# Kernel tuning notes

Hardware: AMD Instinct MI355X
Metric: run time of the kernel (lower is better)

Reference implementation:

```python
import jax, jax.numpy as jnp
import numpy as np

B, NSTEP, NSAMPLE = 16, 32, 10
EMBED, STATE, VOCAB, TOTAL = 128, 512, 32000, 8192
STD_SCALE = 0.113
EPS = 1e-5


def setup_inputs() -> dict:
    key = jax.random.key(0)
    ks = jax.random.split(key, 9)
    g = lambda k, shape: jax.random.normal(k, shape, jnp.float32) * 0.05
    return {
        "zi": jax.random.randint(ks[0], (B,), 0, TOTAL),
        "y": jax.random.randint(ks[1], (B, NSTEP), 0, VOCAB),
        "rd": jax.random.uniform(ks[2], (NSTEP, B, NSAMPLE), jnp.float32),
        "latent": g(ks[3], (TOTAL, EMBED)),
        "state_pref_W": g(ks[4], (STATE, 2 * EMBED)),
        "state_pref_b": g(ks[5], (STATE,)),
        "state_move": g(ks[6], (STATE, EMBED)),
        "vocab_W": g(ks[7], (VOCAB, EMBED)),
        "vocab_b": g(ks[8], (VOCAB,)),
    }


def reference(zi, y, rd, latent, state_pref_W, state_pref_b, state_move, vocab_W, vocab_b):
    # z: [B, NSAMPLE, D] -- latent row per batch element, repeated over samples
    z0 = jnp.repeat(latent[zi][:, None, :], NSAMPLE, axis=1)

    def step(carry, rd_t):
        z, zold, lp = carry
        # per-step normalization (torch std is unbiased, ddof=1)
        z = z / (EPS + jnp.std(z, axis=-1, ddof=1, keepdims=True)) * STD_SCALE
        pref = jnp.concatenate([zold, z], axis=-1) @ state_pref_W.T + state_pref_b  # [B,S,STATE]
        xp = jax.nn.softmax(pref, axis=-1)
        xpc = jnp.cumsum(xp, axis=-1)
        # first index where rd < cumulative prob (argmax of bool = first True)
        which = jnp.argmax(rd_t[:, :, None] < xpc, axis=-1)  # [B,S]
        xps = jnp.take_along_axis(xp, which[:, :, None], axis=-1)[..., 0]
        lp = lp + jnp.log(xps)
        mvs = state_move[which]  # [B,S,D]
        return (z + mvs, z, mvs), mvs

    init = (z0, jnp.zeros_like(z0), jnp.zeros((B, NSAMPLE), jnp.float32))
    # note: carry slot 2 of init is lp=0; fix tuple to match step outputs
    init = (z0, jnp.zeros_like(z0), jnp.zeros((B, NSAMPLE), jnp.float32))

    def step_fixed(carry, rd_t):
        z, zold, lp = carry
        z = z / (EPS + jnp.std(z, axis=-1, ddof=1, keepdims=True)) * STD_SCALE
        pref = jnp.concatenate([zold, z], axis=-1) @ state_pref_W.T + state_pref_b
        xp = jax.nn.softmax(pref, axis=-1)
        xpc = jnp.cumsum(xp, axis=-1)
        which = jnp.argmax(rd_t[:, :, None] < xpc, axis=-1)
        xps = jnp.take_along_axis(xp, which[:, :, None], axis=-1)[..., 0]
        lp = lp + jnp.log(xps)
        mvs = state_move[which]
        return (z + mvs, z, lp), mvs

    (_, _, lp), emits = jax.lax.scan(step_fixed, init, rd)  # emits: [T,B,S,D]
    emits = jnp.transpose(emits, (1, 0, 2, 3))  # [B,T,S,D]
    ys = jax.nn.log_softmax(emits @ vocab_W.T + vocab_b, axis=-1)  # [B,T,S,V]
    idx = jnp.broadcast_to(y[:, :, None, None], (B, NSTEP, NSAMPLE, 1))
    yp = jnp.take_along_axis(ys, idx, axis=-1)[..., 0]  # [B,T,S]
    return yp.mean(axis=2)  # [B,T]
```

## Files before the change

### kernel.cpp

```cpp
#include <hip/hip_runtime.h>
#include <hip/hip_bf16.h>

#define B_ 16
#define T_ 32
#define NS_ 10
#define D_ 128
#define ST_ 512
#define V_ 32000
#define NCHAIN 160

using short8  = __attribute__((ext_vector_type(8))) short;
using f32x4   = __attribute__((ext_vector_type(4))) float;
using half8   = __attribute__((ext_vector_type(8))) _Float16;
using half2v  = __attribute__((ext_vector_type(2))) _Float16;

__device__ __forceinline__ unsigned short f2bf(float f){
  unsigned u = __float_as_uint(f);
  u += 0x7FFFu + ((u >> 16) & 1u);
  return (unsigned short)(u >> 16);
}
__device__ __forceinline__ unsigned packbf(float a, float b){
  return ((unsigned)f2bf(b) << 16) | (unsigned)f2bf(a);
}
__device__ __forceinline__ unsigned short f2h(float f){
  return __builtin_bit_cast(unsigned short, (_Float16)f);
}
__device__ __forceinline__ float h2f(unsigned u, int hi){
  half2v h = __builtin_bit_cast(half2v, u);
  return (float)h[hi];
}
__device__ __forceinline__ float readlane_f(float v, int lane){
  return __int_as_float(__builtin_amdgcn_readlane(__float_as_int(v), lane));
}

#define DPPADD(x, ctrl, rm) { \
  int _t = __builtin_amdgcn_update_dpp(0, __float_as_int(x), ctrl, rm, 0xf, true); \
  x += __int_as_float(_t); }

__global__ __launch_bounds__(256) void prep_kernel(
    const int* __restrict__ zi, const float* __restrict__ latent,
    const float* __restrict__ prefW, const float* __restrict__ move,
    unsigned short* __restrict__ Hh, unsigned short* __restrict__ Lh,
    unsigned short* __restrict__ Gh,
    float* __restrict__ HU0, float* __restrict__ LU0, float* __restrict__ D0,
    float2* __restrict__ S0, float2* __restrict__ SM,
    unsigned* __restrict__ mbf, float* __restrict__ partial)
{
  if (blockIdx.x < 48){
    const int sg = blockIdx.x / 6, vc = blockIdx.x % 6;
    const int wv = threadIdx.x >> 6, lane = threadIdx.x & 63;
    const int c16 = lane & 15, q = lane >> 4;

    half8 afr[4][4];
    #pragma unroll
    for (int rt = 0; rt < 4; ++rt){
      const float* mp = move + (sg*64 + rt*16 + c16)*D_ + q*8;
      #pragma unroll
      for (int kk = 0; kk < 4; ++kk){
        float4 f0 = *(const float4*)(mp + kk*32);
        float4 f1 = *(const float4*)(mp + kk*32 + 4);
        half8 a;
        a[0]=(_Float16)f0.x; a[1]=(_Float16)f0.y; a[2]=(_Float16)f0.z; a[3]=(_Float16)f0.w;
        a[4]=(_Float16)f1.x; a[5]=(_Float16)f1.y; a[6]=(_Float16)f1.z; a[7]=(_Float16)f1.w;
        afr[rt][kk] = a;
      }
    }
    for (int it = 0; it < 4; ++it){
      const int ct = vc*256 + it*64 + wv*16 + c16;
      const float* bp; unsigned short* base; int ccol;
      if (ct < 512)      { bp = prefW + ct*256 + 128; base = Hh; ccol = ct; }
      else if (ct < 1024){ bp = prefW + (ct-512)*256; base = Lh; ccol = ct-512; }
      else               { bp = move + (ct-1024)*128; base = Gh; ccol = ct-1024; }
      half8 bfr[4];
      #pragma unroll
      for (int kk = 0; kk < 4; ++kk){
        float4 f0 = *(const float4*)(bp + q*8 + kk*32);
        float4 f1 = *(const float4*)(bp + q*8 + kk*32 + 4);
        half8 bb;
        bb[0]=(_Float16)f0.x; bb[1]=(_Float16)f0.y; bb[2]=(_Float16)f0.z; bb[3]=(_Float16)f0.w;
        bb[4]=(_Float16)f1.x; bb[5]=(_Float16)f1.y; bb[6]=(_Float16)f1.z; bb[7]=(_Float16)f1.w;
        bfr[kk] = bb;
      }
      #pragma unroll
      for (int rt = 0; rt < 4; ++rt){
        f32x4 acc = {0.f,0.f,0.f,0.f};
        #pragma unroll
        for (int kk = 0; kk < 4; ++kk)
          acc = __builtin_amdgcn_mfma_f32_16x16x32_f16(afr[rt][kk], bfr[kk], acc, 0, 0, 0);
        #pragma unroll
        for (int r = 0; r < 4; ++r){
          const int w = sg*64 + rt*16 + q*4 + r;
          base[w*ST_ + ccol] = f2h(acc[r]);
        }
      }
    }
  } else {
    const int b = blockIdx.x - 48, t = threadIdx.x;
    __shared__ float zl[128];
    if (t < 128) zl[t] = latent[zi[b]*D_ + t];
    __syncthreads();

    #pragma unroll
    for (int ii = 0; ii < 2; ++ii){
      const int sidx = t + ii*256;
      const float* wr = prefW + sidx*256;
      const float* mv = move + sidx*128;
      float hu = 0.f, lu = 0.f, d0 = 0.f;
      #pragma unroll 8
      for (int j = 0; j < 128; j += 4){
        float4 w0 = *(const float4*)(wr + j);
        float4 w1 = *(const float4*)(wr + 128 + j);
        float4 m  = *(const float4*)(mv + j);
        float4 z  = *(const float4*)(&zl[j]);
        lu += w0.x*z.x + w0.y*z.y + w0.z*z.z + w0.w*z.w;
        hu += w1.x*z.x + w1.y*z.y + w1.z*z.z + w1.w*z.w;
        d0 += m.x*z.x + m.y*z.y + m.z*z.z + m.w*z.w;
      }
      HU0[b*ST_ + sidx] = hu; LU0[b*ST_ + sidx] = lu; D0[b*ST_ + sidx] = d0;
    }
    if (t < 64){
      float a = zl[t], bb = zl[t + 64];
      float s1 = a + bb, s2 = a*a + bb*bb;
      #pragma unroll
      for (int m = 1; m < 64; m <<= 1){ s1 += __shfl_xor(s1, m, 64); s2 += __shfl_xor(s2, m, 64); }
      if (t == 0) S0[b] = make_float2(s1, s2);
    }
    {
      const int w = b*32 + (t >> 3);
      const float* mw = move + w*128 + (t & 7)*16;
      float4 m0 = *(const float4*)(mw),   m1 = *(const float4*)(mw+4);
      float4 m2 = *(const float4*)(mw+8), m3 = *(const float4*)(mw+12);
      float s1 = m0.x+m0.y+m0.z+m0.w + m1.x+m1.y+m1.z+m1.w
               + m2.x+m2.y+m2.z+m2.w + m3.x+m3.y+m3.z+m3.w;
      float s2 = m0.x*m0.x+m0.y*m0.y+m0.z*m0.z+m0.w*m0.w
               + m1.x*m1.x+m1.y*m1.y+m1.z*m1.z+m1.w*m1.w
               + m2.x*m2.x+m2.y*m2.y+m2.z*m2.z+m2.w*m2.w
               + m3.x*m3.x+m3.y*m3.y+m3.z*m3.z+m3.w*m3.w;
      #pragma unroll
      for (int m = 1; m < 8; m <<= 1){ s1 += __shfl_xor(s1, m, 64); s2 += __shfl_xor(s2, m, 64); }
      if ((t & 7) == 0) SM[w] = make_float2(s1, s2);
      unsigned* dst = mbf + w*64 + (t & 7)*8;
      dst[0] = packbf(m0.x,m0.y); dst[1] = packbf(m0.z,m0.w);
      dst[2] = packbf(m1.x,m1.y); dst[3] = packbf(m1.z,m1.w);
      dst[4] = packbf(m2.x,m2.y); dst[5] = packbf(m2.z,m2.w);
      dst[6] = packbf(m3.x,m3.y); dst[7] = packbf(m3.z,m3.w);
    }
    if (t < 32) partial[b*32 + t] = 0.f;
  }
}

__global__ __launch_bounds__(256) void work_kernel(
    const unsigned short* __restrict__ Hh, const unsigned short* __restrict__ Lh,
    const unsigned short* __restrict__ Gh, const float2* __restrict__ SM,
    const float* __restrict__ HU0, const float* __restrict__ LU0,
    const float* __restrict__ D0, const float2* __restrict__ S0,
    const float* __restrict__ prefB, const float* __restrict__ rd,
    int* __restrict__ whichOut,
    const unsigned* __restrict__ mbf, const float* __restrict__ vw,
    const float* __restrict__ vb, float* __restrict__ partial)
{
  __shared__ float les[2048];

  if (blockIdx.x < NCHAIN){
    const int t = threadIdx.x;
    if (t >= 64) return;
    const int c = blockIdx.x, b = c / NS_;
    const int l = t, t0 = l*8;

    float HU[8], LU[8], D[8], prev1[8], bias[8];
    #pragma unroll
    for (int k = 0; k < 8; k += 4){
      float4 h = *(const float4*)(HU0 + b*ST_ + t0 + k);
      float4 u = *(const float4*)(LU0 + b*ST_ + t0 + k);
      float4 d = *(const float4*)(D0  + b*ST_ + t0 + k);
      float4 bb= *(const float4*)(prefB + t0 + k);
      HU[k]=h.x; HU[k+1]=h.y; HU[k+2]=h.z; HU[k+3]=h.w;
      LU[k]=u.x; LU[k+1]=u.y; LU[k+2]=u.z; LU[k+3]=u.w;
      D[k]=d.x;  D[k+1]=d.y;  D[k+2]=d.z;  D[k+3]=d.w;
      bias[k]=bb.x; bias[k+1]=bb.y; bias[k+2]=bb.z; bias[k+3]=bb.w;
    }
    #pragma unroll
    for (int k = 0; k < 8; ++k) prev1[k] = 0.f;
    float2 s0 = S0[b];
    float S1 = s0.x, S2 = s0.y;
    float rdreg = (l < T_) ? rd[l*(B_*NS_) + c] : 0.f;

    for (int st = 0; st < T_; ++st){
      const float mean = S1 * (1.f/128.f);
      const float var  = (S2 - 128.f*mean*mean) * (1.f/127.f);
      const float sc   = 0.113f / (1e-5f + sqrtf(var));

      float cum[8]; float run = 0.f;
      #pragma unroll
      for (int k = 0; k < 8; ++k){
        float pref = fmaf(sc, HU[k], prev1[k] + bias[k]);
        run += __expf(pref);
        cum[k] = run;
      }
      float incl = run;
      DPPADD(incl, 0x111, 0xf)
      DPPADD(incl, 0x112, 0xf)
      DPPADD(incl, 0x114, 0xf)
      DPPADD(incl, 0x118, 0xf)
      DPPADD(incl, 0x142, 0xa)
      DPPADD(incl, 0x143, 0xc)
      const float total  = readlane_f(incl, 63);
      const float target = readlane_f(rdreg, st) * total;

      const bool cond = target < incl;
      const unsigned long long bal = __ballot(cond);
      const float excl = incl - run;
      int kw = 7; float dcand = D[7];
      #pragma unroll
      for (int k = 6; k >= 0; --k){
        bool ck = target < excl + cum[k];
        kw = ck ? k : kw;
        dcand = ck ? D[k] : dcand;
      }
      int which; float dW;
      if (bal){
        const int wlane = __ffsll(bal) - 1;
        which = __builtin_amdgcn_readlane(t0 + kw, wlane);
        dW    = readlane_f(dcand, wlane);
      } else {
        which = 0;
        dW    = readlane_f(D[0], 0);
      }
      if (l == 0) whichOut[c*T_ + st] = which;

      const int rb = which*ST_ + t0;
      const uint4 hq = *(const uint4*)(Hh + rb);
      const uint4 lq = *(const uint4*)(Lh + rb);
      const uint4 gq = *(const uint4*)(Gh + rb);
      const float2 sm = SM[which];
      const unsigned ha[4] = {hq.x, hq.y, hq.z, hq.w};
      const unsigned la[4] = {lq.x, lq.y, lq.z, lq.w};
      const unsigned ga[4] = {gq.x, gq.y, gq.z, gq.w};
      #pragma unroll
      for (int k = 0; k < 8; ++k){
        const float Hk = h2f(ha[k>>1], k&1);
        const float Lk = h2f(la[k>>1], k&1);
        const float Gk = h2f(ga[k>>1], k&1);
        const float p1 = sc * LU[k];
        HU[k] = fmaf(sc, HU[k], Hk);
        LU[k] = p1 + Lk;
        D[k]  = fmaf(sc, D[k], Gk);
        prev1[k] = p1;
      }
      S1 = fmaf(sc, S1, sm.x);
      S2 = fmaf(sc*sc, S2, fmaf(2.f*sc, dW, sm.y));
    }
  } else {
    const int t = threadIdx.x, lane = t & 63, wv = t >> 6;
    const int lblk = blockIdx.x - NCHAIN;

    const int vbase = lblk*128 + wv*32;
    short8 afr[2][4];
    float vbr[2][4];
    #pragma unroll
    for (int vt = 0; vt < 2; ++vt){
      const int vr = vbase + vt*16 + (lane & 15);
      const float* wp = vw + vr*D_ + (lane >> 4)*8;
      #pragma unroll
      for (int kk = 0; kk < 4; ++kk){
        float4 f0 = *(const float4*)(wp + kk*32);
        float4 f1 = *(const float4*)(wp + kk*32 + 4);
        short8 a;
        a[0]=(short)f2bf(f0.x); a[1]=(short)f2bf(f0.y);
        a[2]=(short)f2bf(f0.z); a[3]=(short)f2bf(f0.w);
        a[4]=(short)f2bf(f1.x); a[5]=(short)f2bf(f1.y);
        a[6]=(short)f2bf(f1.z); a[7]=(short)f2bf(f1.w);
        afr[vt][kk] = a;
      }
      #pragma unroll
      for (int r = 0; r < 4; ++r)
        vbr[vt][r] = vb[vbase + vt*16 + (lane >> 4)*4 + r];
    }

    const char* mb = (const char*)mbf;
    float esl[32];
    #pragma unroll
    for (int s = 0; s < 32; ++s) esl[s] = 0.f;

    #pragma unroll 4
    for (int s = 0; s < 32; ++s){
      short8 bfr[4];
      #pragma unroll
      for (int kk = 0; kk < 4; ++kk){
        const int row = s*16 + (lane & 15);
        bfr[kk] = *(const short8*)(mb + row*256 + (lane >> 4)*16 + kk*64);
      }
      #pragma unroll
      for (int vt = 0; vt < 2; ++vt){
        f32x4 acc = {0.f,0.f,0.f,0.f};
        #pragma unroll
        for (int kk = 0; kk < 4; ++kk)
          acc = __builtin_amdgcn_mfma_f32_16x16x32_bf16(afr[vt][kk], bfr[kk], acc, 0, 0, 0);
        #pragma unroll
        for (int r = 0; r < 4; ++r)
          esl[s] += __expf(acc[r] + vbr[vt][r]);
      }
    }
    #pragma unroll
    for (int s = 0; s < 32; ++s){
      esl[s] += __shfl_xor(esl[s], 16, 64);
      esl[s] += __shfl_xor(esl[s], 32, 64);
    }
    if (lane < 16){
      #pragma unroll
      for (int s = 0; s < 32; ++s) les[wv*512 + s*16 + lane] = esl[s];
    }
    __syncthreads();
    #pragma unroll
    for (int i = 0; i < 2; ++i){
      const int st = t + i*256;
      atomicAdd(&partial[st], les[st] + les[512+st] + les[1024+st] + les[1536+st]);
    }
  }
}

__global__ __launch_bounds__(256) void dots_kernel(
    const int* __restrict__ whichIn, const int* __restrict__ y,
    const float* __restrict__ move, const float* __restrict__ vw,
    const float* __restrict__ vb, const float* __restrict__ partial,
    float* __restrict__ out)
{
  const int p = blockIdx.x*4 + (threadIdx.x >> 6);
  const int lane = threadIdx.x & 63;
  const int b = p >> 5, st = p & 31;

  int w10 = 0; float ls = 0.f;
  if (lane < NS_){
    w10 = whichIn[(b*NS_ + lane)*T_ + st];
    ls  = __logf(partial[w10]);
  }
  #pragma unroll
  for (int m = 1; m < 16; m <<= 1) ls += __shfl_xor(ls, m, 64);

  float mv0 = 0.f, mv1 = 0.f;
  #pragma unroll
  for (int s = 0; s < NS_; ++s){
    const int ws = __builtin_amdgcn_readlane(w10, s);
    mv0 += move[ws*D_ + lane];
    mv1 += move[ws*D_ + 64 + lane];
  }
  const int yr = y[b*T_ + st];
  float pacc = mv0*vw[yr*D_ + lane] + mv1*vw[yr*D_ + 64 + lane];
  #pragma unroll
  for (int m = 1; m < 64; m <<= 1) pacc += __shfl_xor(pacc, m, 64);
  if (lane == 0) out[b*T_ + st] = (pacc - ls) * (1.f/NS_) + vb[yr];
}

extern "C" void kernel_launch(void* const* d_in, const int* in_sizes, int n_in,
                              void* d_out, int out_size, void* d_ws, size_t ws_size,
                              hipStream_t stream)
{
  const int*   zi     = (const int*)d_in[0];
  const int*   y      = (const int*)d_in[1];
  const float* rd     = (const float*)d_in[2];
  const float* latent = (const float*)d_in[3];
  const float* prefW  = (const float*)d_in[4];
  const float* prefB  = (const float*)d_in[5];
  const float* move   = (const float*)d_in[6];
  const float* vw     = (const float*)d_in[7];
  const float* vb     = (const float*)d_in[8];
  float* out = (float*)d_out;

  char* ws = (char*)d_ws;
  unsigned short* Hh = (unsigned short*)(ws);
  unsigned short* Lh = (unsigned short*)(ws + 524288);
  unsigned short* Gh = (unsigned short*)(ws + 1048576);
  float2* SM    = (float2*)(ws + 1572864);
  float*  HU0   = (float*)(ws + 1576960);
  float*  LU0   = (float*)(ws + 1609728);
  float*  D0    = (float*)(ws + 1642496);
  float2* S0    = (float2*)(ws + 1675264);
  float*  partial = (float*)(ws + 1675392);
  int*    which = (int*)(ws + 1677440);
  unsigned* mbf = (unsigned*)(ws + 1697920);

  hipLaunchKernelGGL(prep_kernel, dim3(64), dim3(256), 0, stream,
                     zi, latent, prefW, move, Hh, Lh, Gh,
                     HU0, LU0, D0, S0, SM, mbf, partial);
  hipLaunchKernelGGL(work_kernel, dim3(NCHAIN + 250), dim3(256), 0, stream,
                     Hh, Lh, Gh, SM, HU0, LU0, D0, S0, prefB, rd, which,
                     mbf, vw, vb, partial);
  hipLaunchKernelGGL(dots_kernel, dim3(128), dim3(256), 0, stream,
                     which, y, move, vw, vb, partial, out);
}
```

Baseline: 65.13 us.

## Fuse dots kernel into work kernel via grid barrier and spread prep GEMM

Merges the final dots kernel into the work kernel using a device-wide atomic barrier, so one launch boundary goes away. The work grid is shrunk to 256 persistent blocks, with 96 blocks looping over the 250 vocab tiles. The prep kernel is split into 192 smaller GEMM blocks instead of 48 so the weight transform spreads across more CUs. The barrier requires all 256 blocks to be co-resident and makes every block spin. Fewer vocab blocks also means less parallelism in the logsumexp phase, which may lengthen it relative to the serial chain.

```diff
diff --git a/kernel.cpp b/kernel.cpp
--- a/kernel.cpp
+++ b/kernel.cpp
@@ -8,6 +8,7 @@
 #define ST_ 512
 #define V_ 32000
 #define NCHAIN 160
+#define NBLK2 256
 
 using short8  = __attribute__((ext_vector_type(8))) short;
 using f32x4   = __attribute__((ext_vector_type(4))) float;
@@ -44,13 +45,15 @@
     unsigned short* __restrict__ Gh,
     float* __restrict__ HU0, float* __restrict__ LU0, float* __restrict__ D0,
     float2* __restrict__ S0, float2* __restrict__ SM,
-    unsigned* __restrict__ mbf, float* __restrict__ partial)
+    unsigned* __restrict__ mbf, float* __restrict__ partial,
+    int* __restrict__ bar)
 {
-  if (blockIdx.x < 48){
-    const int sg = blockIdx.x / 6, vc = blockIdx.x % 6;
-    const int wv = threadIdx.x >> 6, lane = threadIdx.x & 63;
-    const int c16 = lane & 15, q = lane >> 4;
-
+  const int bid = blockIdx.x, t = threadIdx.x;
+  const int lane = t & 63, wv = t >> 6;
+  const int c16 = lane & 15, q = lane >> 4;
+
+  if (bid < 192){
+    const int sg = bid / 24, tile = bid % 24;
     half8 afr[4][4];
     #pragma unroll
     for (int rt = 0; rt < 4; ++rt){
@@ -65,37 +68,35 @@
         afr[rt][kk] = a;
       }
     }
-    for (int it = 0; it < 4; ++it){
-      const int ct = vc*256 + it*64 + wv*16 + c16;
-      const float* bp; unsigned short* base; int ccol;
-      if (ct < 512)      { bp = prefW + ct*256 + 128; base = Hh; ccol = ct; }
-      else if (ct < 1024){ bp = prefW + (ct-512)*256; base = Lh; ccol = ct-512; }
-      else               { bp = move + (ct-1024)*128; base = Gh; ccol = ct-1024; }
-      half8 bfr[4];
-      #pragma unroll
-      for (int kk = 0; kk < 4; ++kk){
-        float4 f0 = *(const float4*)(bp + q*8 + kk*32);
-        float4 f1 = *(const float4*)(bp + q*8 + kk*32 + 4);
-        half8 bb;
-        bb[0]=(_Float16)f0.x; bb[1]=(_Float16)f0.y; bb[2]=(_Float16)f0.z; bb[3]=(_Float16)f0.w;
-        bb[4]=(_Float16)f1.x; bb[5]=(_Float16)f1.y; bb[6]=(_Float16)f1.z; bb[7]=(_Float16)f1.w;
-        bfr[kk] = bb;
-      }
-      #pragma unroll
-      for (int rt = 0; rt < 4; ++rt){
-        f32x4 acc = {0.f,0.f,0.f,0.f};
-        #pragma unroll
-        for (int kk = 0; kk < 4; ++kk)
-          acc = __builtin_amdgcn_mfma_f32_16x16x32_f16(afr[rt][kk], bfr[kk], acc, 0, 0, 0);
-        #pragma unroll
-        for (int r = 0; r < 4; ++r){
-          const int w = sg*64 + rt*16 + q*4 + r;
-          base[w*ST_ + ccol] = f2h(acc[r]);
-        }
+    const int ct = tile*64 + wv*16 + c16;
+    const float* bp; unsigned short* base; int ccol;
+    if (ct < 512)      { bp = prefW + ct*256 + 128; base = Hh; ccol = ct; }
+    else if (ct < 1024){ bp = prefW + (ct-512)*256; base = Lh; ccol = ct-512; }
+    else               { bp = move + (ct-1024)*128; base = Gh; ccol = ct-1024; }
+    half8 bfr[4];
+    #pragma unroll
+    for (int kk = 0; kk < 4; ++kk){
+      float4 f0 = *(const float4*)(bp + q*8 + kk*32);
+      float4 f1 = *(const float4*)(bp + q*8 + kk*32 + 4);
+      half8 bb;
+      bb[0]=(_Float16)f0.x; bb[1]=(_Float16)f0.y; bb[2]=(_Float16)f0.z; bb[3]=(_Float16)f0.w;
+      bb[4]=(_Float16)f1.x; bb[5]=(_Float16)f1.y; bb[6]=(_Float16)f1.z; bb[7]=(_Float16)f1.w;
+      bfr[kk] = bb;
+    }
+    #pragma unroll
+    for (int rt = 0; rt < 4; ++rt){
+      f32x4 acc = {0.f,0.f,0.f,0.f};
+      #pragma unroll
+      for (int kk = 0; kk < 4; ++kk)
+        acc = __builtin_amdgcn_mfma_f32_16x16x32_f16(afr[rt][kk], bfr[kk], acc, 0, 0, 0);
+      #pragma unroll
+      for (int r = 0; r < 4; ++r){
+        const int w = sg*64 + rt*16 + q*4 + r;
+        base[w*ST_ + ccol] = f2h(acc[r]);
       }
     }
   } else {
-    const int b = blockIdx.x - 48, t = threadIdx.x;
+    const int b = bid - 192;
     __shared__ float zl[128];
     if (t < 128) zl[t] = latent[zi[b]*D_ + t];
     __syncthreads();
@@ -146,10 +147,11 @@
       dst[6] = packbf(m3.x,m3.y); dst[7] = packbf(m3.z,m3.w);
     }
     if (t < 32) partial[b*32 + t] = 0.f;
+    if (b == 0 && t == 64) *bar = 0;
   }
 }
 
-__global__ __launch_bounds__(256) void work_kernel(
+__global__ __launch_bounds__(256) void workdots_kernel(
     const unsigned short* __restrict__ Hh, const unsigned short* __restrict__ Lh,
     const unsigned short* __restrict__ Gh, const float2* __restrict__ SM,
     const float* __restrict__ HU0, const float* __restrict__ LU0,
@@ -157,198 +159,207 @@
     const float* __restrict__ prefB, const float* __restrict__ rd,
     int* __restrict__ whichOut,
     const unsigned* __restrict__ mbf, const float* __restrict__ vw,
-    const float* __restrict__ vb, float* __restrict__ partial)
+    const float* __restrict__ vb, float* __restrict__ partial,
+    const int* __restrict__ y, const float* __restrict__ move,
+    float* __restrict__ out, int* __restrict__ bar)
 {
   __shared__ float les[2048];
-
-  if (blockIdx.x < NCHAIN){
-    const int t = threadIdx.x;
-    if (t >= 64) return;
-    const int c = blockIdx.x, b = c / NS_;
-    const int l = t, t0 = l*8;
-
-    float HU[8], LU[8], D[8], prev1[8], bias[8];
-    #pragma unroll
-    for (int k = 0; k < 8; k += 4){
-      float4 h = *(const float4*)(HU0 + b*ST_ + t0 + k);
-      float4 u = *(const float4*)(LU0 + b*ST_ + t0 + k);
-      float4 d = *(const float4*)(D0  + b*ST_ + t0 + k);
-      float4 bb= *(const float4*)(prefB + t0 + k);
-      HU[k]=h.x; HU[k+1]=h.y; HU[k+2]=h.z; HU[k+3]=h.w;
-      LU[k]=u.x; LU[k+1]=u.y; LU[k+2]=u.z; LU[k+3]=u.w;
-      D[k]=d.x;  D[k+1]=d.y;  D[k+2]=d.z;  D[k+3]=d.w;
-      bias[k]=bb.x; bias[k+1]=bb.y; bias[k+2]=bb.z; bias[k+3]=bb.w;
-    }
-    #pragma unroll
-    for (int k = 0; k < 8; ++k) prev1[k] = 0.f;
-    float2 s0 = S0[b];
-    float S1 = s0.x, S2 = s0.y;
-    float rdreg = (l < T_) ? rd[l*(B_*NS_) + c] : 0.f;
-
-    for (int st = 0; st < T_; ++st){
-      const float mean = S1 * (1.f/128.f);
-      const float var  = (S2 - 128.f*mean*mean) * (1.f/127.f);
-      const float sc   = 0.113f / (1e-5f + sqrtf(var));
-
-      float cum[8]; float run = 0.f;
-      #pragma unroll
-      for (int k = 0; k < 8; ++k){
-        float pref = fmaf(sc, HU[k], prev1[k] + bias[k]);
-        run += __expf(pref);
-        cum[k] = run;
-      }
-      float incl = run;
-      DPPADD(incl, 0x111, 0xf)
-      DPPADD(incl, 0x112, 0xf)
-      DPPADD(incl, 0x114, 0xf)
-      DPPADD(incl, 0x118, 0xf)
-      DPPADD(incl, 0x142, 0xa)
-      DPPADD(incl, 0x143, 0xc)
-      const float total  = readlane_f(incl, 63);
-      const float target = readlane_f(rdreg, st) * total;
-
-      const bool cond = target < incl;
-      const unsigned long long bal = __ballot(cond);
-      const float excl = incl - run;
-      int kw = 7; float dcand = D[7];
-      #pragma unroll
-      for (int k = 6; k >= 0; --k){
-        bool ck = target < excl + cum[k];
-        kw = ck ? k : kw;
-        dcand = ck ? D[k] : dcand;
-      }
-      int which; float dW;
-      if (bal){
-        const int wlane = __ffsll(bal) - 1;
-        which = __builtin_amdgcn_readlane(t0 + kw, wlane);
-        dW    = readlane_f(dcand, wlane);
-      } else {
-        which = 0;
-        dW    = readlane_f(D[0], 0);
-      }
-      if (l == 0) whichOut[c*T_ + st] = which;
-
-      const int rb = which*ST_ + t0;
-      const uint4 hq = *(const uint4*)(Hh + rb);
-      const uint4 lq = *(const uint4*)(Lh + rb);
-      const uint4 gq = *(const uint4*)(Gh + rb);
-      const float2 sm = SM[which];
-      const unsigned ha[4] = {hq.x, hq.y, hq.z, hq.w};
-      const unsigned la[4] = {lq.x, lq.y, lq.z, lq.w};
-      const unsigned ga[4] = {gq.x, gq.y, gq.z, gq.w};
-      #pragma unroll
-      for (int k = 0; k < 8; ++k){
-        const float Hk = h2f(ha[k>>1], k&1);
-        const float Lk = h2f(la[k>>1], k&1);
-        const float Gk = h2f(ga[k>>1], k&1);
-        const float p1 = sc * LU[k];
-        HU[k] = fmaf(sc, HU[k], Hk);
-        LU[k] = p1 + Lk;
-        D[k]  = fmaf(sc, D[k], Gk);
-        prev1[k] = p1;
-      }
-      S1 = fmaf(sc, S1, sm.x);
-      S2 = fmaf(sc*sc, S2, fmaf(2.f*sc, dW, sm.y));
+  const int bid = blockIdx.x, t = threadIdx.x;
+  const int lane = t & 63, wv = t >> 6;
+  const int c16 = lane & 15, q = lane >> 4;
+
+  if (bid < NCHAIN){
+    if (t < 64){
+      const int c = bid, b = c / NS_;
+      const int l = t, t0 = l*8;
+
+      float HU[8], LU[8], D[8], prev1[8], bias[8];
+      #pragma unroll
+      for (int k = 0; k < 8; k += 4){
+        float4 h = *(const float4*)(HU0 + b*ST_ + t0 + k);
+        float4 u = *(const float4*)(LU0 + b*ST_ + t0 + k);
+        float4 d = *(const float4*)(D0  + b*ST_ + t0 + k);
+        float4 bb= *(const float4*)(prefB + t0 + k);
+        HU[k]=h.x; HU[k+1]=h.y; HU[k+2]=h.z; HU[k+3]=h.w;
+        LU[k]=u.x; LU[k+1]=u.y; LU[k+2]=u.z; LU[k+3]=u.w;
+        D[k]=d.x;  D[k+1]=d.y;  D[k+2]=d.z;  D[k+3]=d.w;
+        bias[k]=bb.x; bias[k+1]=bb.y; bias[k+2]=bb.z; bias[k+3]=bb.w;
+      }
+      #pragma unroll
+      for (int k = 0; k < 8; ++k) prev1[k] = 0.f;
+      float2 s0 = S0[b];
+      float S1 = s0.x, S2 = s0.y;
+      float rdreg = (l < T_) ? rd[l*(B_*NS_) + c] : 0.f;
+
+      for (int st = 0; st < T_; ++st){
+        const float mean = S1 * (1.f/128.f);
+        const float var  = (S2 - 128.f*mean*mean) * (1.f/127.f);
+        const float sc   = 0.113f / (1e-5f + sqrtf(var));
+
+        float cum[8]; float run = 0.f;
+        #pragma unroll
+        for (int k = 0; k < 8; ++k){
+          float pref = fmaf(sc, HU[k], prev1[k] + bias[k]);
+          run += __expf(pref);
+          cum[k] = run;
+        }
+        float incl = run;
+        DPPADD(incl, 0x111, 0xf)
+        DPPADD(incl, 0x112, 0xf)
+        DPPADD(incl, 0x114, 0xf)
+        DPPADD(incl, 0x118, 0xf)
+        DPPADD(incl, 0x142, 0xa)
+        DPPADD(incl, 0x143, 0xc)
+        const float total  = readlane_f(incl, 63);
+        const float target = readlane_f(rdreg, st) * total;
+
+        const bool cond = target < incl;
+        const unsigned long long bal = __ballot(cond);
+        const float excl = incl - run;
+        int kw = 7; float dcand = D[7];
+        #pragma unroll
+        for (int k = 6; k >= 0; --k){
+          bool ck = target < excl + cum[k];
+          kw = ck ? k : kw;
+          dcand = ck ? D[k] : dcand;
+        }
+        int which; float dW;
+        if (bal){
+          const int wlane = __ffsll(bal) - 1;
+          which = __builtin_amdgcn_readlane(t0 + kw, wlane);
+          dW    = readlane_f(dcand, wlane);
+        } else {
+          which = 0;
+          dW    = readlane_f(D[0], 0);
+        }
+        if (l == 0) whichOut[c*T_ + st] = which;
+
+        const int rb = which*ST_ + t0;
+        const uint4 hq = *(const uint4*)(Hh + rb);
+        const uint4 lq = *(const uint4*)(Lh + rb);
+        const uint4 gq = *(const uint4*)(Gh + rb);
+        const float2 sm = SM[which];
+        const unsigned ha[4] = {hq.x, hq.y, hq.z, hq.w};
+        const unsigned la[4] = {lq.x, lq.y, lq.z, lq.w};
+        const unsigned ga[4] = {gq.x, gq.y, gq.z, gq.w};
+        #pragma unroll
+        for (int k = 0; k < 8; ++k){
+          const float Hk = h2f(ha[k>>1], k&1);
+          const float Lk = h2f(la[k>>1], k&1);
+          const float Gk = h2f(ga[k>>1], k&1);
+          const float p1 = sc * LU[k];
+          HU[k] = fmaf(sc, HU[k], Hk);
+          LU[k] = p1 + Lk;
+          D[k]  = fmaf(sc, D[k], Gk);
+          prev1[k] = p1;
+        }
+        S1 = fmaf(sc, S1, sm.x);
+        S2 = fmaf(sc*sc, S2, fmaf(2.f*sc, dW, sm.y));
+      }
     }
   } else {
-    const int t = threadIdx.x, lane = t & 63, wv = t >> 6;
-    const int lblk = blockIdx.x - NCHAIN;
-
-    const int vbase = lblk*128 + wv*32;
-    short8 afr[2][4];
-    float vbr[2][4];
-    #pragma unroll
-    for (int vt = 0; vt < 2; ++vt){
-      const int vr = vbase + vt*16 + (lane & 15);
-      const float* wp = vw + vr*D_ + (lane >> 4)*8;
-      #pragma unroll
-      for (int kk = 0; kk < 4; ++kk){
-        float4 f0 = *(const float4*)(wp + kk*32);
-        float4 f1 = *(const float4*)(wp + kk*32 + 4);
-        short8 a;
-        a[0]=(short)f2bf(f0.x); a[1]=(short)f2bf(f0.y);
-        a[2]=(short)f2bf(f0.z); a[3]=(short)f2bf(f0.w);
-        a[4]=(short)f2bf(f1.x); a[5]=(short)f2bf(f1.y);
-        a[6]=(short)f2bf(f1.z); a[7]=(short)f2bf(f1.w);
-        afr[vt][kk] = a;
-      }
-      #pragma unroll
-      for (int r = 0; r < 4; ++r)
-        vbr[vt][r] = vb[vbase + vt*16 + (lane >> 4)*4 + r];
-    }
-
     const char* mb = (const char*)mbf;
-    float esl[32];
-    #pragma unroll
-    for (int s = 0; s < 32; ++s) esl[s] = 0.f;
-
-    #pragma unroll 4
-    for (int s = 0; s < 32; ++s){
-      short8 bfr[4];
-      #pragma unroll
-      for (int kk = 0; kk < 4; ++kk){
-        const int row = s*16 + (lane & 15);
-        bfr[kk] = *(const short8*)(mb + row*256 + (lane >> 4)*16 + kk*64);
-      }
+    for (int u = bid - NCHAIN; u < 250; u += NBLK2 - NCHAIN){
+      const int vbase = u*128 + wv*32;
+      short8 afr[2][4];
+      float vbr[2][4];
       #pragma unroll
       for (int vt = 0; vt < 2; ++vt){
-        f32x4 acc = {0.f,0.f,0.f,0.f};
-        #pragma unroll
-        for (int kk = 0; kk < 4; ++kk)
-          acc = __builtin_amdgcn_mfma_f32_16x16x32_bf16(afr[vt][kk], bfr[kk], acc, 0, 0, 0);
+        const int vr = vbase + vt*16 + c16;
+        const float* wp = vw + vr*D_ + q*8;
+        #pragma unroll
+        for (int kk = 0; kk < 4; ++kk){
+          float4 f0 = *(const float4*)(wp + kk*32);
+          float4 f1 = *(const float4*)(wp + kk*32 + 4);
+          short8 a;
+          a[0]=(short)f2bf(f0.x); a[1]=(short)f2bf(f0.y);
+          a[2]=(short)f2bf(f0.z); a[3]=(short)f2bf(f0.w);
+          a[4]=(short)f2bf(f1.x); a[5]=(short)f2bf(f1.y);
+          a[6]=(short)f2bf(f1.z); a[7]=(short)f2bf(f1.w);
+          afr[vt][kk] = a;
+        }
         #pragma unroll
         for (int r = 0; r < 4; ++r)
-          esl[s] += __expf(acc[r] + vbr[vt][r]);
-      }
-    }
-    #pragma unroll
-    for (int s = 0; s < 32; ++s){
-      esl[s] += __shfl_xor(esl[s], 16, 64);
-      esl[s] += __shfl_xor(esl[s], 32, 64);
-    }
-    if (lane < 16){
-      #pragma unroll
-      for (int s = 0; s < 32; ++s) les[wv*512 + s*16 + lane] = esl[s];
-    }
-    __syncthreads();
-    #pragma unroll
-    for (int i = 0; i < 2; ++i){
-      const int st = t + i*256;
-      atomicAdd(&partial[st], les[st] + les[512+st] + les[1024+st] + les[1536+st]);
+          vbr[vt][r] = vb[vbase + vt*16 + q*4 + r];
+      }
+
+      float esl[32];
+      #pragma unroll
+      for (int s = 0; s < 32; ++s) esl[s] = 0.f;
+
+      #pragma unroll
+      for (int s = 0; s < 32; ++s){
+        short8 bfr[4];
+        #pragma unroll
+        for (int kk = 0; kk < 4; ++kk){
+          const int row = s*16 + c16;
+          bfr[kk] = *(const short8*)(mb + row*256 + q*16 + kk*64);
+        }
+        #pragma unroll
+        for (int vt = 0; vt < 2; ++vt){
+          f32x4 acc = {0.f,0.f,0.f,0.f};
+          #pragma unroll
+          for (int kk = 0; kk < 4; ++kk)
+            acc = __builtin_amdgcn_mfma_f32_16x16x32_bf16(afr[vt][kk], bfr[kk], acc, 0, 0, 0);
+          #pragma unroll
+          for (int r = 0; r < 4; ++r)
+            esl[s] += __expf(acc[r] + vbr[vt][r]);
+        }
+      }
+      #pragma unroll
+      for (int s = 0; s < 32; ++s){
+        esl[s] += __shfl_xor(esl[s], 16, 64);
+        esl[s] += __shfl_xor(esl[s], 32, 64);
+      }
+      if (lane < 16){
+        #pragma unroll
+        for (int s = 0; s < 32; ++s) les[wv*512 + s*16 + lane] = esl[s];
+      }
+      __syncthreads();
+      #pragma unroll
+      for (int i = 0; i < 2; ++i){
+        const int st = t + i*256;
+        atomicAdd(&partial[st], les[st] + les[512+st] + les[1024+st] + les[1536+st]);
+      }
+      __syncthreads();
     }
   }
-}
-
-__global__ __launch_bounds__(256) void dots_kernel(
-    const int* __restrict__ whichIn, const int* __restrict__ y,
-    const float* __restrict__ move, const float* __restrict__ vw,
-    const float* __restrict__ vb, const float* __restrict__ partial,
-    float* __restrict__ out)
-{
-  const int p = blockIdx.x*4 + (threadIdx.x >> 6);
-  const int lane = threadIdx.x & 63;
-  const int b = p >> 5, st = p & 31;
-
-  int w10 = 0; float ls = 0.f;
-  if (lane < NS_){
-    w10 = whichIn[(b*NS_ + lane)*T_ + st];
-    ls  = __logf(partial[w10]);
+
+  __syncthreads();
+  if (t == 0){
+    __threadfence();
+    __hip_atomic_fetch_add(bar, 1, __ATOMIC_ACQ_REL, __HIP_MEMORY_SCOPE_AGENT);
+    while (__hip_atomic_load(bar, __ATOMIC_ACQUIRE, __HIP_MEMORY_SCOPE_AGENT) < NBLK2)
+      __builtin_amdgcn_s_sleep(2);
   }
-  #pragma unroll
-  for (int m = 1; m < 16; m <<= 1) ls += __shfl_xor(ls, m, 64);
-
-  float mv0 = 0.f, mv1 = 0.f;
-  #pragma unroll
-  for (int s = 0; s < NS_; ++s){
-    const int ws = __builtin_amdgcn_readlane(w10, s);
-    mv0 += move[ws*D_ + lane];
-    mv1 += move[ws*D_ + 64 + lane];
+  __syncthreads();
+  __threadfence();
+
+  if (bid < 128){
+    const int p = bid*4 + wv;
+    const int b = p >> 5, st = p & 31;
+
+    int w10 = 0; float ls = 0.f;
+    if (lane < NS_){
+      w10 = whichOut[(b*NS_ + lane)*T_ + st];
+      ls  = __logf(partial[w10]);
+    }
+    #pragma unroll
+    for (int m = 1; m < 16; m <<= 1) ls += __shfl_xor(ls, m, 64);
+
+    float mv0 = 0.f, mv1 = 0.f;
+    #pragma unroll
+    for (int s = 0; s < NS_; ++s){
+      const int ws = __builtin_amdgcn_readlane(w10, s);
+      mv0 += move[ws*D_ + lane];
+      mv1 += move[ws*D_ + 64 + lane];
+    }
+    const int yr = y[b*T_ + st];
+    float pacc = mv0*vw[yr*D_ + lane] + mv1*vw[yr*D_ + 64 + lane];
+    #pragma unroll
+    for (int m = 1; m < 64; m <<= 1) pacc += __shfl_xor(pacc, m, 64);
+    if (lane == 0) out[b*T_ + st] = (pacc - ls) * (1.f/NS_) + vb[yr];
   }
-  const int yr = y[b*T_ + st];
-  float pacc = mv0*vw[yr*D_ + lane] + mv1*vw[yr*D_ + 64 + lane];
-  #pragma unroll
-  for (int m = 1; m < 64; m <<= 1) pacc += __shfl_xor(pacc, m, 64);
-  if (lane == 0) out[b*T_ + st] = (pacc - ls) * (1.f/NS_) + vb[yr];
 }
 
 extern "C" void kernel_launch(void* const* d_in, const int* in_sizes, int n_in,
@@ -378,13 +389,12 @@
   float*  partial = (float*)(ws + 1675392);
   int*    which = (int*)(ws + 1677440);
   unsigned* mbf = (unsigned*)(ws + 1697920);
-
-  hipLaunchKernelGGL(prep_kernel, dim3(64), dim3(256), 0, stream,
+  int*    bar   = (int*)(ws + 1828992);
+
+  hipLaunchKernelGGL(prep_kernel, dim3(208), dim3(256), 0, stream,
                      zi, latent, prefW, move, Hh, Lh, Gh,
-                     HU0, LU0, D0, S0, SM, mbf, partial);
-  hipLaunchKernelGGL(work_kernel, dim3(NCHAIN + 250), dim3(256), 0, stream,
+                     HU0, LU0, D0, S0, SM, mbf, partial, bar);
+  hipLaunchKernelGGL(workdots_kernel, dim3(NBLK2), dim3(256), 0, stream,
                      Hh, Lh, Gh, SM, HU0, LU0, D0, S0, prefB, rd, which,
-                     mbf, vw, vb, partial);
-  hipLaunchKernelGGL(dots_kernel, dim3(128), dim3(256), 0, stream,
-                     which, y, move, vw, vb, partial, out);
-}
+                     mbf, vw, vb, partial, y, move, out, bar);
+}
```

Result: slower. 168.0 us (+158.0%).
